# Performance work log

Hardware: AMD Instinct MI355X
Metric: run time of the kernel (lower is better)

## Reference

```python
import jax, jax.numpy as jnp
import numpy as np

B, S, D, L, R = 8, 128, 512, 512, 50  # batch, seq_len, input_dim, linear_dim, n_rel_labels


def _head_params(key, n_out):
    k1, k2, k3, k4 = jax.random.split(key, 4)
    s1 = 1.0 / np.sqrt(2 * D)
    s2 = 1.0 / np.sqrt(L)
    return (jax.random.uniform(k1, (2 * D, L), jnp.float32, -s1, s1),
            jax.random.uniform(k2, (L,), jnp.float32, -s1, s1),
            jax.random.uniform(k3, (L, n_out), jnp.float32, -s2, s2),
            jax.random.uniform(k4, (n_out,), jnp.float32, -s2, s2))


def setup_inputs() -> dict:
    key = jax.random.key(0)
    kx, ks, kh, kt, kl = jax.random.split(key, 5)
    x = jax.random.normal(kx, (B, S, D), jnp.float32)
    span = _head_params(ks, 1)
    h2h = _head_params(kh, 1)
    t2t = _head_params(kt, 1)
    lab = _head_params(kl, R)
    return {
        'x': x,
        'span_W1': span[0], 'span_b1': span[1], 'span_W2': span[2], 'span_b2': span[3],
        'h2h_W1': h2h[0], 'h2h_b1': h2h[1], 'h2h_W2': h2h[2], 'h2h_b2': h2h[3],
        't2t_W1': t2t[0], 't2t_b1': t2t[1], 't2t_W2': t2t[2], 't2t_b2': t2t[3],
        'lab_W1': lab[0], 'lab_b1': lab[1], 'lab_W2': lab[2], 'lab_b2': lab[3],
    }


def _pair_head(x, W1, b1, W2, b2):
    # Linear on concat([x_i, x_j]) == x_i @ W_left + x_j @ W_right  (avoids [B,S,S,2D] concat)
    d = x.shape[-1]
    Wl, Wr = W1[:d], W1[d:]
    left = jnp.einsum('bid,dl->bil', x, Wl)   # [B,S,L]
    right = jnp.einsum('bjd,dl->bjl', x, Wr)  # [B,S,L]
    h = jnp.tanh(left[:, :, None, :] + right[:, None, :, :] + b1)  # [B,S,S,L]
    return jnp.einsum('bijl,lo->bijo', h, W2) + b2  # [B,S,S,n_out]


def reference(x, span_W1, span_b1, span_W2, span_b2,
              h2h_W1, h2h_b1, h2h_W2, h2h_b2,
              t2t_W1, t2t_b1, t2t_W2, t2t_b2,
              lab_W1, lab_b1, lab_W2, lab_b2):
    shst = _pair_head(x, span_W1, span_b1, span_W2, span_b2)[..., 0]  # [B,S,S]
    # torch: movedim(-1,1) -> triu + triu(1).T -> movedim(1,-1)
    bt = jnp.swapaxes(shst, 1, 2)
    sym = jnp.triu(bt) + jnp.swapaxes(jnp.triu(bt, 1), -1, -2)
    shst = jnp.swapaxes(sym, 1, 2)
    shoh = _pair_head(x, h2h_W1, h2h_b1, h2h_W2, h2h_b2)[..., 0]
    stot = _pair_head(x, t2t_W1, t2t_b1, t2t_W2, t2t_b2)[..., 0]
    shoh_labels = _pair_head(x, lab_W1, lab_b1, lab_W2, lab_b2)  # [B,S,S,R]
    return (shst, shoh, stot, shoh_labels)
```

## Files before the change

### kernel.cpp

```cpp
#include <hip/hip_runtime.h>

#define Bsz 8
#define Ssz 128
#define Dsz 512
#define D2 1024
#define Lsz 512
#define Rsz 50
#define SLOT 524288
#define BSLOT 65536
#define OUTMAT 131072

typedef __attribute__((ext_vector_type(8))) _Float16 f16x8;
typedef __attribute__((ext_vector_type(2))) __fp16 fp16x2;
typedef __attribute__((ext_vector_type(4))) float f32x4;

union UV4 { uint4 u; f16x8 h; };
union UH { unsigned short s; _Float16 h; };
union UP { fp16x2 h; unsigned u; };

struct K1Args {
  const float* W1[4];
  const float* b1[4];
};

__device__ __forceinline__ float f16lo(unsigned u) {
  UH x; x.s = (unsigned short)(u & 0xffffu); return (float)x.h;
}
__device__ __forceinline__ float f16hi(unsigned u) {
  UH x; x.s = (unsigned short)(u >> 16); return (float)x.h;
}
__device__ __forceinline__ unsigned pkrtz(float a, float b) {
  UP c; c.h = __builtin_amdgcn_cvt_pkrtz(a, b); return c.u;
}
__device__ __forceinline__ unsigned short f2h(float v) {
  UH x; x.h = (_Float16)v; return x.s;
}
__device__ __forceinline__ float rcpf(float x) {
  return __builtin_amdgcn_rcpf(x);
}

__global__ __launch_bounds__(256) void prep_all(
    const float* __restrict__ x, K1Args a, const float* __restrict__ W2,
    unsigned short* __restrict__ W1F, unsigned short* __restrict__ X16F,
    unsigned short* __restrict__ W2F) {
  const int z = blockIdx.z;
  const int t = threadIdx.x;
  if (z < 4) {
    if (blockIdx.x >= 8) return;
    __shared__ float S[64][65];
    const float* __restrict__ W = a.W1[z];
    const int n0 = blockIdx.x * 64;
    const int k0 = blockIdx.y * 64;
    {
      const int kk = t >> 2, c16 = (t & 3) * 16;
      const float* p = W + (k0 + kk) * Lsz + n0 + c16;
#pragma unroll
      for (int c = 0; c < 4; ++c) {
        float4 v = *(const float4*)(p + c * 4);
        S[kk][c16 + c * 4 + 0] = v.x; S[kk][c16 + c * 4 + 1] = v.y;
        S[kk][c16 + c * 4 + 2] = v.z; S[kk][c16 + c * 4 + 3] = v.w;
      }
    }
    __syncthreads();
#pragma unroll
    for (int o = t; o < 512; o += 256) {
      const int lane = o & 63;
      const int ntl = (o >> 6) & 3, kbl = o >> 8;
      const int n_l = ntl * 16 + (lane & 15);
      const int k_l = kbl * 32 + (lane >> 4) * 8;
      uint4 pk;
      pk.x = pkrtz(S[k_l + 0][n_l], S[k_l + 1][n_l]);
      pk.y = pkrtz(S[k_l + 2][n_l], S[k_l + 3][n_l]);
      pk.z = pkrtz(S[k_l + 4][n_l], S[k_l + 5][n_l]);
      pk.w = pkrtz(S[k_l + 6][n_l], S[k_l + 7][n_l]);
      const long addr =
          ((long)((z * 32 + blockIdx.x * 4 + ntl) * 32 + blockIdx.y * 2 + kbl) *
               64 + lane) * 8;
      *(uint4*)(W1F + addr) = pk;
    }
  } else if (z == 4) {
    const int idx = (blockIdx.y * 16 + blockIdx.x) * 256 + t;
    const int frag = idx >> 6, lane = idx & 63;
    const int m = (frag >> 4) * 16 + (lane & 15);
    const int k0 = (frag & 15) * 32 + (lane >> 4) * 8;
    const float* p = x + m * Dsz + k0;
    float4 v0 = *(const float4*)p, v1 = *(const float4*)(p + 4);
    uint4 pk = make_uint4(pkrtz(v0.x, v0.y), pkrtz(v0.z, v0.w),
                          pkrtz(v1.x, v1.y), pkrtz(v1.z, v1.w));
    *(uint4*)(X16F + (long)idx * 8) = pk;
  } else {
    if (blockIdx.y != 0 || blockIdx.x >= 16) return;
    const int idx = blockIdx.x * 256 + t;
    const int frag = idx >> 6, lane = idx & 63;
    const int o = (frag >> 4) * 16 + (lane & 15);
    const int k0 = (frag & 15) * 32 + (lane >> 4) * 8;
    float v[8];
#pragma unroll
    for (int e = 0; e < 8; ++e)
      v[e] = (o < Rsz) ? W2[(k0 + e) * Rsz + o] : 0.0f;
    uint4 pk = make_uint4(pkrtz(v[0], v[1]), pkrtz(v[2], v[3]),
                          pkrtz(v[4], v[5]), pkrtz(v[6], v[7]));
    *(uint4*)(W2F + (long)idx * 8) = pk;
  }
}

__global__ __launch_bounds__(256) void gemm_lr_f16f(
    const unsigned short* __restrict__ X16F,
    const unsigned short* __restrict__ W1F, K1Args a,
    unsigned short* __restrict__ U) {
  const int side = blockIdx.z;
  const int h = side >> 1, r = side & 1;
  const float* __restrict__ bias = a.b1[h];
  const int tid = threadIdx.x;
  const int w = tid >> 6, lane = tid & 63;
  const int lm = lane & 15, q = lane >> 4;
  const int mtb = blockIdx.y * 4 + (w & 1) * 2;
  const int ntb = blockIdx.x * 4 + (w >> 1) * 2;

  f32x4 acc[2][2];
#pragma unroll
  for (int mt = 0; mt < 2; ++mt)
#pragma unroll
    for (int nt = 0; nt < 2; ++nt) {
      acc[mt][nt].x = 0.f; acc[mt][nt].y = 0.f;
      acc[mt][nt].z = 0.f; acc[mt][nt].w = 0.f;
    }

  for (int kb = 0; kb < 16; ++kb) {
    UV4 af[2], bf[2];
#pragma unroll
    for (int mt = 0; mt < 2; ++mt)
      af[mt].u = *(const uint4*)(X16F +
          ((long)((mtb + mt) * 16 + kb) * 64 + lane) * 8);
#pragma unroll
    for (int nt = 0; nt < 2; ++nt)
      bf[nt].u = *(const uint4*)(W1F +
          ((long)((h * 32 + ntb + nt) * 32 + r * 16 + kb) * 64 + lane) * 8);
#pragma unroll
    for (int mt = 0; mt < 2; ++mt)
#pragma unroll
      for (int nt = 0; nt < 2; ++nt)
        acc[mt][nt] = __builtin_amdgcn_mfma_f32_16x16x32_f16(
            af[mt].h, bf[nt].h, acc[mt][nt], 0, 0, 0);
  }

  unsigned short* slot = U + side * SLOT;
  if (h < 3) {
#pragma unroll
    for (int nt = 0; nt < 2; ++nt) {
      const int n_out = (ntb + nt) * 16 + lm;
      const float bb = (r == 0) ? bias[n_out] : 0.0f;
#pragma unroll
      for (int mt = 0; mt < 2; ++mt) {
        const int m0r = (mtb + mt) * 16 + q * 4;
        const float e0 = __expf(2.0f * (acc[mt][nt].x + bb));
        const float e1 = __expf(2.0f * (acc[mt][nt].y + bb));
        const float e2 = __expf(2.0f * (acc[mt][nt].z + bb));
        const float e3 = __expf(2.0f * (acc[mt][nt].w + bb));
        uint2 pr;
        pr.x = pkrtz(e0, e1);
        pr.y = pkrtz(e2, e3);
        const int bi = m0r >> 7, il = m0r & 127;
        *(uint2*)(slot + bi * BSLOT + n_out * Ssz + il) = pr;
      }
    }
  } else {
#pragma unroll
    for (int nt = 0; nt < 2; ++nt) {
      const int n_out = (ntb + nt) * 16 + lm;
      const float bb = (r == 0) ? bias[n_out] : 0.0f;
#pragma unroll
      for (int mt = 0; mt < 2; ++mt) {
#pragma unroll
        for (int reg = 0; reg < 4; ++reg) {
          const int m_out = (mtb + mt) * 16 + q * 4 + reg;
          float v;
          if (reg == 0) v = acc[mt][nt].x;
          else if (reg == 1) v = acc[mt][nt].y;
          else if (reg == 2) v = acc[mt][nt].z;
          else v = acc[mt][nt].w;
          slot[m_out * Lsz + n_out] = f2h(__expf(2.0f * (v + bb)));
        }
      }
    }
  }
}

__global__ __launch_bounds__(256) void pair_scalar5(
    const unsigned short* __restrict__ U,
    const float* __restrict__ w2a, const float* __restrict__ w2b,
    const float* __restrict__ w2c, float* __restrict__ P) {
  const int zh = blockIdx.z;
  const int h = zh >> 1, half = zh & 1;
  const int b = blockIdx.y;
  const int it = blockIdx.x >> 2, jt = blockIdx.x & 3;
  if (h == 0 && jt > it) return;
  const int i0 = it * 32, j0 = jt * 32;
  const int t = threadIdx.x;
  const int tj = t & 15, ti = t >> 4;

  const unsigned short* __restrict__ A  = U + (2 * h) * SLOT + b * BSLOT;
  const unsigned short* __restrict__ Bt = U + (2 * h + 1) * SLOT + b * BSLOT;
  const float* __restrict__ w2 = (h == 0) ? w2a : (h == 1 ? w2b : w2c);

  __shared__ unsigned short Ls[64][40];
  __shared__ unsigned short Rs[64][40];
  __shared__ float w2s[64];

  float acc00 = 0.f, acc01 = 0.f, acc10 = 0.f, acc11 = 0.f;
  const int sr = t >> 2;
  const int sc = (t & 3) * 8;
  const int lbase = half * 256;

  for (int lc = 0; lc < 256; lc += 64) {
    __syncthreads();
    const int gl = lbase + lc + sr;
    *(uint4*)&Ls[sr][sc] = *(const uint4*)(A + gl * Ssz + i0 + sc);
    *(uint4*)&Rs[sr][sc] = *(const uint4*)(Bt + gl * Ssz + j0 + sc);
    if (t < 64) w2s[t] = w2[lbase + lc + t];
    __syncthreads();
#pragma unroll 4
    for (int l = 0; l < 64; ++l) {
      const unsigned ua = *(const unsigned*)&Ls[l][ti * 2];
      const unsigned ub = *(const unsigned*)&Rs[l][tj * 2];
      const float ax = f16lo(ua), ay = f16hi(ua);
      const float bx = f16lo(ub), by = f16hi(ub);
      const float wv = w2s[l];
      acc00 = fmaf(wv, rcpf(fmaf(ax, bx, 1.0f)), acc00);
      acc01 = fmaf(wv, rcpf(fmaf(ax, by, 1.0f)), acc01);
      acc10 = fmaf(wv, rcpf(fmaf(ay, bx, 1.0f)), acc10);
      acc11 = fmaf(wv, rcpf(fmaf(ay, by, 1.0f)), acc11);
    }
  }

  float* Pp = P + ((long)(zh * Bsz + b)) * 16384;
  const int i = i0 + ti * 2, j = j0 + tj * 2;
  *(float2*)&Pp[(i + 0) * Ssz + j] = make_float2(acc00, acc01);
  *(float2*)&Pp[(i + 1) * Ssz + j] = make_float2(acc10, acc11);
}

__global__ __launch_bounds__(128) void combine_scalar(
    const float* __restrict__ P,
    const float* __restrict__ w2a, const float* __restrict__ w2b,
    const float* __restrict__ w2c,
    const float* __restrict__ b2a, const float* __restrict__ b2b,
    const float* __restrict__ b2c,
    float* __restrict__ out) {
  const int h = blockIdx.z;
  const int b = blockIdx.y;
  const int i = blockIdx.x;
  const int t = threadIdx.x;
  const float* __restrict__ w2 = (h == 0) ? w2a : (h == 1 ? w2b : w2c);
  const float bias = (h == 0) ? b2a[0] : (h == 1 ? b2b[0] : b2c[0]);

  __shared__ float red[128];
  float s = w2[t] + w2[t + 128] + w2[t + 256] + w2[t + 384];
  red[t] = s;
  __syncthreads();
  if (t < 64) red[t] += red[t + 64];
  __syncthreads();
  if (t < 32) red[t] += red[t + 32];
  __syncthreads();
  if (t < 16) red[t] += red[t + 16];
  __syncthreads();
  if (t < 8) red[t] += red[t + 8];
  __syncthreads();
  if (t < 4) red[t] += red[t + 4];
  __syncthreads();
  if (t < 2) red[t] += red[t + 2];
  __syncthreads();
  const float S = red[0] + red[1];

  const float* P0 = P + ((long)(h * 2 * Bsz + b)) * 16384;
  const float* P1 = P + ((long)((h * 2 + 1) * Bsz + b)) * 16384;
  int ii = i, jj = t;
  if (h == 0 && t > i) { ii = t; jj = i; }
  const float p = P0[ii * Ssz + jj] + P1[ii * Ssz + jj];
  out[h * OUTMAT + (b * Ssz + i) * Ssz + t] = S - 2.0f * p + bias;
}

__global__ __launch_bounds__(256) void pair_label8(
    const unsigned short* __restrict__ U,
    const unsigned short* __restrict__ W2F,
    const float* __restrict__ b2, float* __restrict__ out) {
  const int b = blockIdx.y;
  const int i = blockIdx.x;
  const int tid = threadIdx.x;
  const int w = tid >> 6, lane = tid & 63;
  const int lm = lane & 15, q = lane >> 4;
  const int jb = w * 32;

  const unsigned short* __restrict__ Lrow = U + 6 * SLOT + (b * Ssz + i) * Lsz;
  const unsigned short* __restrict__ Rb0 = U + 7 * SLOT + (long)b * Ssz * Lsz;
  float* out3 = out + 3 * OUTMAT;

  __shared__ unsigned short Rs[2][128][68];
  __shared__ unsigned short Bs[2][8][512];

  const int sr = tid >> 1;
  const int sh = (tid & 1) * 32;
  const unsigned short* Rg = Rb0 + sr * Lsz + sh;
  const int bfrag = tid >> 5;
  const int bo = (tid & 31) * 16;
  const int fragN = (bfrag & 3) * 16 + (bfrag >> 2);

  f32x4 acc[2][4];
#pragma unroll
  for (int mt = 0; mt < 2; ++mt)
#pragma unroll
    for (int nt = 0; nt < 4; ++nt) {
      acc[mt][nt].x = 0.f; acc[mt][nt].y = 0.f;
      acc[mt][nt].z = 0.f; acc[mt][nt].w = 0.f;
    }

  uint4 rp0, rp1, rp2, rp3, bp0, bp1;
  {
    const unsigned short* p = Rg;
    rp0 = *(const uint4*)(p);      rp1 = *(const uint4*)(p + 8);
    rp2 = *(const uint4*)(p + 16); rp3 = *(const uint4*)(p + 24);
    const unsigned short* bp = W2F + (long)fragN * 512 + bo;
    bp0 = *(const uint4*)(bp);     bp1 = *(const uint4*)(bp + 8);
  }
  *(uint4*)&Rs[0][sr][sh + 0]  = rp0;
  *(uint4*)&Rs[0][sr][sh + 8]  = rp1;
  *(uint4*)&Rs[0][sr][sh + 16] = rp2;
  *(uint4*)&Rs[0][sr][sh + 24] = rp3;
  *(uint4*)&Bs[0][bfrag][bo]     = bp0;
  *(uint4*)&Bs[0][bfrag][bo + 8] = bp1;
  __syncthreads();

#pragma unroll 1
  for (int c = 0; c < 8; ++c) {
    const int buf = c & 1;
    if (c < 7) {
      const unsigned short* p = Rg + (c + 1) * 64;
      rp0 = *(const uint4*)(p);      rp1 = *(const uint4*)(p + 8);
      rp2 = *(const uint4*)(p + 16); rp3 = *(const uint4*)(p + 24);
      const unsigned short* bp = W2F + (long)(fragN + (c + 1) * 2) * 512 + bo;
      bp0 = *(const uint4*)(bp);     bp1 = *(const uint4*)(bp + 8);
    }
    const uint4 lf0 = *(const uint4*)(Lrow + c * 64 + q * 8);
    const uint4 lf1 = *(const uint4*)(Lrow + c * 64 + 32 + q * 8);

#pragma unroll
    for (int kbl = 0; kbl < 2; ++kbl) {
      const uint4 lf = kbl ? lf1 : lf0;
      float ea[8];
      ea[0] = f16lo(lf.x); ea[1] = f16hi(lf.x);
      ea[2] = f16lo(lf.y); ea[3] = f16hi(lf.y);
      ea[4] = f16lo(lf.z); ea[5] = f16hi(lf.z);
      ea[6] = f16lo(lf.w); ea[7] = f16hi(lf.w);
      UV4 bfr[4];
#pragma unroll
      for (int nt = 0; nt < 4; ++nt)
        bfr[nt].u = *(const uint4*)&Bs[buf][kbl * 4 + nt][lane * 8];
#pragma unroll
      for (int mt = 0; mt < 2; ++mt) {
        const uint4 rv =
            *(const uint4*)&Rs[buf][jb + mt * 16 + lm][kbl * 32 + q * 8];
        float eb[8];
        eb[0] = f16lo(rv.x); eb[1] = f16hi(rv.x);
        eb[2] = f16lo(rv.y); eb[3] = f16hi(rv.y);
        eb[4] = f16lo(rv.z); eb[5] = f16hi(rv.z);
        eb[6] = f16lo(rv.w); eb[7] = f16hi(rv.w);
        float hh[8];
#pragma unroll
        for (int e = 0; e < 8; ++e)
          hh[e] = fmaf(-2.0f, rcpf(fmaf(ea[e], eb[e], 1.0f)), 1.0f);
        UV4 A;
        A.u = make_uint4(pkrtz(hh[0], hh[1]), pkrtz(hh[2], hh[3]),
                         pkrtz(hh[4], hh[5]), pkrtz(hh[6], hh[7]));
#pragma unroll
        for (int nt = 0; nt < 4; ++nt)
          acc[mt][nt] = __builtin_amdgcn_mfma_f32_16x16x32_f16(
              A.h, bfr[nt].h, acc[mt][nt], 0, 0, 0);
      }
    }
    if (c < 7) {
      const int nb = buf ^ 1;
      *(uint4*)&Rs[nb][sr][sh + 0]  = rp0;
      *(uint4*)&Rs[nb][sr][sh + 8]  = rp1;
      *(uint4*)&Rs[nb][sr][sh + 16] = rp2;
      *(uint4*)&Rs[nb][sr][sh + 24] = rp3;
      *(uint4*)&Bs[nb][bfrag][bo]     = bp0;
      *(uint4*)&Bs[nb][bfrag][bo + 8] = bp1;
    }
    __syncthreads();
  }

#pragma unroll
  for (int nt = 0; nt < 4; ++nt) {
    const int o = nt * 16 + lm;
    if (o >= Rsz) continue;
    const float bias = b2[o];
#pragma unroll
    for (int mt = 0; mt < 2; ++mt) {
#pragma unroll
      for (int reg = 0; reg < 4; ++reg) {
        const int j = jb + mt * 16 + q * 4 + reg;
        const long base = ((long)((b * Ssz + i) * Ssz) + j) * Rsz;
        float v;
        if (reg == 0) v = acc[mt][nt].x;
        else if (reg == 1) v = acc[mt][nt].y;
        else if (reg == 2) v = acc[mt][nt].z;
        else v = acc[mt][nt].w;
        out3[base + o] = v + bias;
      }
    }
  }
}

extern "C" void kernel_launch(void* const* d_in, const int* in_sizes, int n_in,
                              void* d_out, int out_size, void* d_ws,
                              size_t ws_size, hipStream_t stream) {
  (void)in_sizes; (void)n_in; (void)out_size; (void)ws_size;
  const float* x = (const float*)d_in[0];
  K1Args a;
  a.W1[0] = (const float*)d_in[1];  a.b1[0] = (const float*)d_in[2];
  a.W1[1] = (const float*)d_in[5];  a.b1[1] = (const float*)d_in[6];
  a.W1[2] = (const float*)d_in[9];  a.b1[2] = (const float*)d_in[10];
  a.W1[3] = (const float*)d_in[13]; a.b1[3] = (const float*)d_in[14];
  const float* w2a = (const float*)d_in[3];
  const float* b2a = (const float*)d_in[4];
  const float* w2b = (const float*)d_in[7];
  const float* b2b = (const float*)d_in[8];
  const float* w2c = (const float*)d_in[11];
  const float* b2c = (const float*)d_in[12];
  const float* W2l = (const float*)d_in[15];
  const float* b2l = (const float*)d_in[16];
  float* out = (float*)d_out;

  unsigned short* U    = (unsigned short*)d_ws;
  unsigned short* W1F  = U + 8 * SLOT;
  unsigned short* X16F = U + 8 * SLOT + 4 * (Lsz * D2);
  unsigned short* W2F  = U + 8 * SLOT + 5 * (Lsz * D2);
  float* P = (float*)W1F;

  prep_all<<<dim3(16, 16, 6), 256, 0, stream>>>(x, a, W2l, W1F, X16F, W2F);
  gemm_lr_f16f<<<dim3(8, 16, 8), 256, 0, stream>>>(X16F, W1F, a, U);
  pair_scalar5<<<dim3(16, Bsz, 6), 256, 0, stream>>>(U, w2a, w2b, w2c, P);
  combine_scalar<<<dim3(Ssz, Bsz, 3), 128, 0, stream>>>(
      P, w2a, w2b, w2c, b2a, b2b, b2c, out);
  pair_label8<<<dim3(Ssz, Bsz), 256, 0, stream>>>(U, W2F, b2l, out);
}
```

Measured before the change: 168.7 us.

## Fuse scalar-head combine into pair kernel and precompute W2 sums in prep

```diff
diff --git a/kernel.cpp b/kernel.cpp
--- a/kernel.cpp
+++ b/kernel.cpp
@@ -29,6 +29,9 @@
 __device__ __forceinline__ float f16hi(unsigned u) {
   UH x; x.s = (unsigned short)(u >> 16); return (float)x.h;
 }
+__device__ __forceinline__ float f16v(unsigned short s) {
+  UH x; x.s = s; return (float)x.h;
+}
 __device__ __forceinline__ unsigned pkrtz(float a, float b) {
   UP c; c.h = __builtin_amdgcn_cvt_pkrtz(a, b); return c.u;
 }
@@ -41,8 +44,12 @@
 
 __global__ __launch_bounds__(256) void prep_all(
     const float* __restrict__ x, K1Args a, const float* __restrict__ W2,
+    const float* __restrict__ w2a, const float* __restrict__ w2b,
+    const float* __restrict__ w2c,
+    const float* __restrict__ b2a, const float* __restrict__ b2b,
+    const float* __restrict__ b2c,
     unsigned short* __restrict__ W1F, unsigned short* __restrict__ X16F,
-    unsigned short* __restrict__ W2F) {
+    unsigned short* __restrict__ W2F, float* __restrict__ Sums) {
   const int z = blockIdx.z;
   const int t = threadIdx.x;
   if (z < 4) {
@@ -79,6 +86,7 @@
       *(uint4*)(W1F + addr) = pk;
     }
   } else if (z == 4) {
+    if (blockIdx.x >= 16) return;
     const int idx = (blockIdx.y * 16 + blockIdx.x) * 256 + t;
     const int frag = idx >> 6, lane = idx & 63;
     const int m = (frag >> 4) * 16 + (lane & 15);
@@ -89,18 +97,32 @@
                           pkrtz(v1.x, v1.y), pkrtz(v1.z, v1.w));
     *(uint4*)(X16F + (long)idx * 8) = pk;
   } else {
-    if (blockIdx.y != 0 || blockIdx.x >= 16) return;
-    const int idx = blockIdx.x * 256 + t;
-    const int frag = idx >> 6, lane = idx & 63;
-    const int o = (frag >> 4) * 16 + (lane & 15);
-    const int k0 = (frag & 15) * 32 + (lane >> 4) * 8;
-    float v[8];
-#pragma unroll
-    for (int e = 0; e < 8; ++e)
-      v[e] = (o < Rsz) ? W2[(k0 + e) * Rsz + o] : 0.0f;
-    uint4 pk = make_uint4(pkrtz(v[0], v[1]), pkrtz(v[2], v[3]),
-                          pkrtz(v[4], v[5]), pkrtz(v[6], v[7]));
-    *(uint4*)(W2F + (long)idx * 8) = pk;
+    if (blockIdx.y != 0) return;
+    if (blockIdx.x < 16) {
+      const int idx = blockIdx.x * 256 + t;
+      const int frag = idx >> 6, lane = idx & 63;
+      const int o = (frag >> 4) * 16 + (lane & 15);
+      const int k0 = (frag & 15) * 32 + (lane >> 4) * 8;
+      float v[8];
+#pragma unroll
+      for (int e = 0; e < 8; ++e)
+        v[e] = (o < Rsz) ? W2[(k0 + e) * Rsz + o] : 0.0f;
+      uint4 pk = make_uint4(pkrtz(v[0], v[1]), pkrtz(v[2], v[3]),
+                            pkrtz(v[4], v[5]), pkrtz(v[6], v[7]));
+      *(uint4*)(W2F + (long)idx * 8) = pk;
+    } else if (blockIdx.x < 19) {
+      const int h = blockIdx.x - 16;
+      const float* __restrict__ w2 = (h == 0) ? w2a : (h == 1 ? w2b : w2c);
+      const float bb = (h == 0) ? b2a[0] : (h == 1 ? b2b[0] : b2c[0]);
+      __shared__ float red[256];
+      red[t] = w2[t] + w2[t + 256];
+      __syncthreads();
+      for (int s = 128; s > 0; s >>= 1) {
+        if (t < s) red[t] += red[t + s];
+        __syncthreads();
+      }
+      if (t == 0) Sums[h] = red[0] + bb;
+    }
   }
 }
 
@@ -186,97 +208,68 @@
   }
 }
 
-__global__ __launch_bounds__(256) void pair_scalar5(
+__global__ __launch_bounds__(256) void pair_scalar6(
     const unsigned short* __restrict__ U,
     const float* __restrict__ w2a, const float* __restrict__ w2b,
-    const float* __restrict__ w2c, float* __restrict__ P) {
-  const int zh = blockIdx.z;
-  const int h = zh >> 1, half = zh & 1;
+    const float* __restrict__ w2c, const float* __restrict__ Sums,
+    float* __restrict__ out) {
+  const int h = blockIdx.z;
   const int b = blockIdx.y;
   const int it = blockIdx.x >> 2, jt = blockIdx.x & 3;
-  if (h == 0 && jt > it) return;
-  const int i0 = it * 32, j0 = jt * 32;
+  const int i0 = it * 16, j0 = jt * 32;
+  if (h == 0 && i0 + 15 < j0) return;
   const int t = threadIdx.x;
-  const int tj = t & 15, ti = t >> 4;
+  const int tj = t & 31;
+  const int th = t >> 5;
 
   const unsigned short* __restrict__ A  = U + (2 * h) * SLOT + b * BSLOT;
   const unsigned short* __restrict__ Bt = U + (2 * h + 1) * SLOT + b * BSLOT;
   const float* __restrict__ w2 = (h == 0) ? w2a : (h == 1 ? w2b : w2c);
 
-  __shared__ unsigned short Ls[64][40];
-  __shared__ unsigned short Rs[64][40];
+  __shared__ unsigned short As[64][20];
+  __shared__ unsigned short Bs[64][40];
   __shared__ float w2s[64];
 
-  float acc00 = 0.f, acc01 = 0.f, acc10 = 0.f, acc11 = 0.f;
+  float acc0 = 0.f, acc1 = 0.f;
   const int sr = t >> 2;
-  const int sc = (t & 3) * 8;
-  const int lbase = half * 256;
-
-  for (int lc = 0; lc < 256; lc += 64) {
+  const int scA = (t & 3) * 4;
+  const int scB = (t & 3) * 8;
+
+  for (int lc = 0; lc < Lsz; lc += 64) {
     __syncthreads();
-    const int gl = lbase + lc + sr;
-    *(uint4*)&Ls[sr][sc] = *(const uint4*)(A + gl * Ssz + i0 + sc);
-    *(uint4*)&Rs[sr][sc] = *(const uint4*)(Bt + gl * Ssz + j0 + sc);
-    if (t < 64) w2s[t] = w2[lbase + lc + t];
+    *(uint2*)&As[sr][scA] = *(const uint2*)(A + (lc + sr) * Ssz + i0 + scA);
+    *(uint4*)&Bs[sr][scB] = *(const uint4*)(Bt + (lc + sr) * Ssz + j0 + scB);
+    if (t < 64) w2s[t] = w2[lc + t];
     __syncthreads();
-#pragma unroll 4
+#pragma unroll 8
     for (int l = 0; l < 64; ++l) {
-      const unsigned ua = *(const unsigned*)&Ls[l][ti * 2];
-      const unsigned ub = *(const unsigned*)&Rs[l][tj * 2];
-      const float ax = f16lo(ua), ay = f16hi(ua);
-      const float bx = f16lo(ub), by = f16hi(ub);
       const float wv = w2s[l];
-      acc00 = fmaf(wv, rcpf(fmaf(ax, bx, 1.0f)), acc00);
-      acc01 = fmaf(wv, rcpf(fmaf(ax, by, 1.0f)), acc01);
-      acc10 = fmaf(wv, rcpf(fmaf(ay, bx, 1.0f)), acc10);
-      acc11 = fmaf(wv, rcpf(fmaf(ay, by, 1.0f)), acc11);
-    }
-  }
-
-  float* Pp = P + ((long)(zh * Bsz + b)) * 16384;
-  const int i = i0 + ti * 2, j = j0 + tj * 2;
-  *(float2*)&Pp[(i + 0) * Ssz + j] = make_float2(acc00, acc01);
-  *(float2*)&Pp[(i + 1) * Ssz + j] = make_float2(acc10, acc11);
-}
-
-__global__ __launch_bounds__(128) void combine_scalar(
-    const float* __restrict__ P,
-    const float* __restrict__ w2a, const float* __restrict__ w2b,
-    const float* __restrict__ w2c,
-    const float* __restrict__ b2a, const float* __restrict__ b2b,
-    const float* __restrict__ b2c,
-    float* __restrict__ out) {
-  const int h = blockIdx.z;
-  const int b = blockIdx.y;
-  const int i = blockIdx.x;
-  const int t = threadIdx.x;
-  const float* __restrict__ w2 = (h == 0) ? w2a : (h == 1 ? w2b : w2c);
-  const float bias = (h == 0) ? b2a[0] : (h == 1 ? b2b[0] : b2c[0]);
-
-  __shared__ float red[128];
-  float s = w2[t] + w2[t + 128] + w2[t + 256] + w2[t + 384];
-  red[t] = s;
-  __syncthreads();
-  if (t < 64) red[t] += red[t + 64];
-  __syncthreads();
-  if (t < 32) red[t] += red[t + 32];
-  __syncthreads();
-  if (t < 16) red[t] += red[t + 16];
-  __syncthreads();
-  if (t < 8) red[t] += red[t + 8];
-  __syncthreads();
-  if (t < 4) red[t] += red[t + 4];
-  __syncthreads();
-  if (t < 2) red[t] += red[t + 2];
-  __syncthreads();
-  const float S = red[0] + red[1];
-
-  const float* P0 = P + ((long)(h * 2 * Bsz + b)) * 16384;
-  const float* P1 = P + ((long)((h * 2 + 1) * Bsz + b)) * 16384;
-  int ii = i, jj = t;
-  if (h == 0 && t > i) { ii = t; jj = i; }
-  const float p = P0[ii * Ssz + jj] + P1[ii * Ssz + jj];
-  out[h * OUTMAT + (b * Ssz + i) * Ssz + t] = S - 2.0f * p + bias;
+      const unsigned ua = *(const unsigned*)&As[l][th * 2];
+      const float a0 = f16lo(ua), a1 = f16hi(ua);
+      const float bb = f16v(Bs[l][tj]);
+      acc0 = fmaf(wv, rcpf(fmaf(a0, bb, 1.0f)), acc0);
+      acc1 = fmaf(wv, rcpf(fmaf(a1, bb, 1.0f)), acc1);
+    }
+  }
+
+  const float Sh = Sums[h];
+  const float v0 = fmaf(-2.0f, acc0, Sh);
+  const float v1 = fmaf(-2.0f, acc1, Sh);
+  const int i = i0 + th * 2, j = j0 + tj;
+  if (h == 0) {
+    if (j <= i) {
+      out[(b * Ssz + i) * Ssz + j] = v0;
+      out[(b * Ssz + j) * Ssz + i] = v0;
+    }
+    if (j <= i + 1) {
+      out[(b * Ssz + i + 1) * Ssz + j] = v1;
+      out[(b * Ssz + j) * Ssz + (i + 1)] = v1;
+    }
+  } else {
+    float* o = out + h * OUTMAT;
+    o[(b * Ssz + i) * Ssz + j] = v0;
+    o[(b * Ssz + i + 1) * Ssz + j] = v1;
+  }
 }
 
 __global__ __launch_bounds__(256) void pair_label8(
@@ -434,12 +427,12 @@
   unsigned short* W1F  = U + 8 * SLOT;
   unsigned short* X16F = U + 8 * SLOT + 4 * (Lsz * D2);
   unsigned short* W2F  = U + 8 * SLOT + 5 * (Lsz * D2);
-  float* P = (float*)W1F;
-
-  prep_all<<<dim3(16, 16, 6), 256, 0, stream>>>(x, a, W2l, W1F, X16F, W2F);
+  float* Sums = (float*)(W2F + 64 * Lsz);
+
+  prep_all<<<dim3(19, 16, 6), 256, 0, stream>>>(
+      x, a, W2l, w2a, w2b, w2c, b2a, b2b, b2c, W1F, X16F, W2F, Sums);
   gemm_lr_f16f<<<dim3(8, 16, 8), 256, 0, stream>>>(X16F, W1F, a, U);
-  pair_scalar5<<<dim3(16, Bsz, 6), 256, 0, stream>>>(U, w2a, w2b, w2c, P);
-  combine_scalar<<<dim3(Ssz, Bsz, 3), 128, 0, stream>>>(
-      P, w2a, w2b, w2c, b2a, b2b, b2c, out);
   pair_label8<<<dim3(Ssz, Bsz), 256, 0, stream>>>(U, W2F, b2l, out);
-}
+  pair_scalar6<<<dim3(32, Bsz, 3), 256, 0, stream>>>(
+      U, w2a, w2b, w2c, Sums, out);
+}
```

Measured after the change: 166.4 us. About the same (-1.4%).
